# Performance work log

Hardware: AMD Instinct MI355X
Metric: run time of the kernel (lower is better)

## Reference

```python
import jax, jax.numpy as jnp
import numpy as np

# Production-scale dims (see shape_source)
B, C, H, W = 4, 128, 64, 64
RADIUS = 0.2
TEMP = 0.1
PAD_VALUE = 0.0
P = int(H * RADIUS) * 2 + 1  # local window size kH = kW = 25


def setup_inputs() -> dict:
    key = jax.random.key(0)
    k1, k2 = jax.random.split(key)
    query = jax.random.normal(k1, (B, C, H, W), dtype=jnp.float32)
    keys = jax.random.normal(k2, (B, C, H, W), dtype=jnp.float32)
    return {"query": query, "keys": keys}


def _make_idx_map(h_dim, w_dim, p):
    # Equivalent of F.unfold(arange(H*W).view(H,W), kernel=(P,P), pad=P//2).clamp(min=0)
    # idx[h, w, p1, p2] = linear index of (h+p1-P//2, w+p2-P//2), 0 if out of bounds
    off = np.arange(p) - p // 2
    hh = np.arange(h_dim)[:, None, None, None] + off[None, None, :, None]  # (H,1,P,1)
    ww = np.arange(w_dim)[None, :, None, None] + off[None, None, None, :]  # (1,W,1,P)
    valid = (hh >= 0) & (hh < h_dim) & (ww >= 0) & (ww < w_dim)
    idx = np.where(valid, hh * w_dim + ww, 0)  # (H,W,P,P)
    return jnp.asarray(idx.reshape(h_dim * w_dim, p * p), dtype=jnp.int32)

_IDX_MAP = _make_idx_map(H, W, P)  # (H*W, P*P) int32 constant


def _local_correlation(query, keys, p):
    # spatial_correlation_sample(kernel=1, patch=P, stride=1, pad=0, dilation=1):
    # att[b,p1,p2,h,w] = sum_c query[b,c,h,w] * keys_zero_padded[b,c,h+p1-P//2,w+p2-P//2]
    pad = p // 2
    keys_pad = jnp.pad(keys, ((0, 0), (0, 0), (pad, pad), (pad, pad)))

    def corr_one(i):
        p1, p2 = i // p, i % p
        k = jax.lax.dynamic_slice(keys_pad, (0, 0, p1, p2), keys.shape)
        return jnp.einsum('bchw,bchw->bhw', query, k)

    att = jax.lax.map(corr_one, jnp.arange(p * p))  # (P*P, B, H, W); sequential keeps memory low
    return jnp.transpose(att, (1, 2, 3, 0))  # b h w (p1 p2)


def reference(query, keys):
    n_pix = H * W
    att = _local_correlation(query, keys, P) / TEMP  # (B,H,W,P*P)
    # knn(): pad_value==0, topk==0 -> mask exact zeros (out-of-window zero-padded corrs) to -10
    A = jnp.where(att == PAD_VALUE, jnp.float32(-10.0), att)
    A = jnp.exp(A.reshape(B, n_pix, P * P))  # b (h w) n
    # scatter_add into dense (B, H*W, H*W) affinity map
    q_idx = jnp.arange(n_pix)[:, None]  # (HW,1)
    out = jnp.zeros((B, n_pix, n_pix), dtype=A.dtype)
    out = out.at[:, q_idx, _IDX_MAP].add(A)
    # rearr 'b (h w) n -> b n h w'
    return out.reshape(B, H, W, n_pix).transpose(0, 3, 1, 2)
```

## Files before the change

kernel.cpp:

```cpp
#include <hip/hip_runtime.h>
#include <math.h>


#define BDIM 256
constexpr int Bn = 4, Cc = 128, Hh = 64, Ww = 64, HW = 4096;
constexpr int P = 25, Rr = 12, T = 8;

__device__ __forceinline__ int cntf(int x) {
    int c = P;
    if (x < Rr) c -= (Rr - x);
    if (x > (Hh - 1 - Rr)) c -= (x - (Hh - 1 - Rr));
    return c;
}

__global__ __launch_bounds__(BDIM, 6) void localwalk_kernel(
    const float* __restrict__ query, const float* __restrict__ keys,
    float* __restrict__ out)
{
    const int jt = blockIdx.x;
    const int jh = blockIdx.y;
    const int b  = blockIdx.z;
    const int jw0 = jt * T;
    const int t = threadIdx.x;

    __shared__ float S[T * P * P];

    const float E10 = expf(-10.0f);
    const bool special = (jh == 0) && (jt == 0);

    const float* kb = keys + (size_t)b * Cc * HW + jh * Ww + jw0;
    for (int i = t; i < Cc * T; i += BDIM)
        S[i] = kb[(size_t)(i >> 3) * HW + (i & 7)];
    __syncthreads();

    const int wg   = t & 7;
    const int hloc = t >> 3;
    const int h  = jh - Rr + hloc;
    const int hA = min(max(h, 0), Hh - 1);
    const int w0 = jw0 - Rr + wg * 4;
    const int wA0 = min(max(w0, 0), Ww - 4);
    const bool wgv = (w0 >= 0) && (w0 + 3 < Ww);
    const bool hok = (hloc < P) && (h >= 0) && (h < Hh);

    float acc[4][T];
    #pragma unroll
    for (int ww = 0; ww < 4; ++ww)
        #pragma unroll
        for (int jj = 0; jj < T; ++jj) acc[ww][jj] = 0.f;

    const float* qp = query + (size_t)b * Cc * HW + hA * Ww + wA0;

#define STEPQ(QREG, CIDX) do {                                            \
        float4 k0_ = *(const float4*)&S[(CIDX) * 8];                      \
        float4 k1_ = *(const float4*)&S[(CIDX) * 8 + 4];                  \
        float kk_[T] = {k0_.x, k0_.y, k0_.z, k0_.w,                       \
                        k1_.x, k1_.y, k1_.z, k1_.w};                      \
        float qq_[4] = {(QREG).x, (QREG).y, (QREG).z, (QREG).w};          \
        _Pragma("unroll")                                                 \
        for (int jj_ = 0; jj_ < T; ++jj_)                                 \
            _Pragma("unroll")                                             \
            for (int ww_ = 0; ww_ < 4; ++ww_)                             \
                acc[ww_][jj_] = fmaf(qq_[ww_], kk_[jj_], acc[ww_][jj_]);  \
    } while (0)
#define LOADQ(QREG, CIDX) (QREG) = *(const float4*)(qp + (size_t)(CIDX) * HW)

    float4 q0, q1, q2, q3;
    LOADQ(q0, 0); LOADQ(q1, 1); LOADQ(q2, 2); LOADQ(q3, 3);

    for (int c0 = 0; c0 < Cc - 4; c0 += 4) {
        STEPQ(q0, c0 + 0); LOADQ(q0, c0 + 4);
        STEPQ(q1, c0 + 1); LOADQ(q1, c0 + 5);
        STEPQ(q2, c0 + 2); LOADQ(q2, c0 + 6);
        STEPQ(q3, c0 + 3); LOADQ(q3, c0 + 7);
    }
    STEPQ(q0, Cc - 4); STEPQ(q1, Cc - 3); STEPQ(q2, Cc - 2); STEPQ(q3, Cc - 1);

#undef STEPQ
#undef LOADQ

    __syncthreads();

    if (hok && wgv) {
        #pragma unroll
        for (int jj = 0; jj < T; ++jj) {
            #pragma unroll
            for (int ww = 0; ww < 4; ++ww) {
                const int d = wg * 4 + ww - jj;
                if ((unsigned)d < (unsigned)P) {
                    float att = acc[ww][jj] / 0.1f;
                    if (att == 0.0f) att = -10.0f;
                    att = fminf(att, 88.0f);
                    S[(jj * P + hloc) * P + d] = expf(att);
                }
            }
        }
    }
    __syncthreads();

    float4* orow4 = (float4*)(out + ((size_t)(b * HW + jh * Ww + jw0)) * HW);
    for (int k = 0; k < 32; ++k) {
        int fi = t + k * BDIM;
        int jj  = fi >> 10;
        int idx = fi & 1023;
        int hh  = idx >> 4;
        int w4  = (idx & 15) * 4;
        int hl  = hh - (jh - Rr);
        bool hin = (hl >= 0) && (hl < P);

        float4 v = make_float4(0.f, 0.f, 0.f, 0.f);
        if (special && jj == 0) {
            int ch = cntf(hh);
            v.x = (float)(P * P - ch * cntf(w4 + 0)) * E10;
            v.y = (float)(P * P - ch * cntf(w4 + 1)) * E10;
            v.z = (float)(P * P - ch * cntf(w4 + 2)) * E10;
            v.w = (float)(P * P - ch * cntf(w4 + 3)) * E10;
        }
        if (hin) {
            int base = (jj * P + hl) * P;
            int off  = jw0 + jj - Rr;
            int we0  = w4 - off;
            if ((unsigned)(we0 + 0) < (unsigned)P) v.x += S[base + we0 + 0];
            if ((unsigned)(we0 + 1) < (unsigned)P) v.y += S[base + we0 + 1];
            if ((unsigned)(we0 + 2) < (unsigned)P) v.z += S[base + we0 + 2];
            if ((unsigned)(we0 + 3) < (unsigned)P) v.w += S[base + we0 + 3];
        }
        orow4[fi] = v;
    }
}

extern "C" void kernel_launch(void* const* d_in, const int* in_sizes, int n_in,
                              void* d_out, int out_size, void* d_ws, size_t ws_size,
                              hipStream_t stream) {
    const float* query = (const float*)d_in[0];
    const float* keys  = (const float*)d_in[1];
    float* out = (float*)d_out;
    dim3 grid(Ww / T, Hh, Bn);
    localwalk_kernel<<<grid, dim3(BDIM), 0, stream>>>(query, keys, out);
}
```

Measured before the change: 354.8 us.

## Process two column tiles per block, overlapping first tile's stores with second tile's compute

Each block now handles 16 query columns as two 8-column tiles. It interleaves the dense output writes of the first tile with the channel-reduction loop of the second tile, so global stores can overlap FMA work. The grid is halved and the occupancy hint drops from 6 to 4. Exchanged for this are more shared memory per block (a key tile buffer of 128×16 floats) and fewer blocks in flight.

```diff
diff --git a/kernel.cpp b/kernel.cpp
--- a/kernel.cpp
+++ b/kernel.cpp
@@ -13,46 +13,69 @@
     return c;
 }
 
-__global__ __launch_bounds__(BDIM, 6) void localwalk_kernel(
+__device__ __forceinline__ void d_chunk(int k, int t, int jh, int jw0s, bool sp,
+                                        const float* __restrict__ S,
+                                        float4* __restrict__ orow4, float E10)
+{
+    int fi  = t + k * BDIM;
+    int jj  = fi >> 10;
+    int idx = fi & 1023;
+    int hh  = idx >> 4;
+    int w4  = (idx & 15) * 4;
+    int hl  = hh - (jh - Rr);
+    bool hin = (hl >= 0) && (hl < P);
+
+    float4 v = make_float4(0.f, 0.f, 0.f, 0.f);
+    if (sp && jj == 0) {
+        int ch = cntf(hh);
+        v.x = (float)(P * P - ch * cntf(w4 + 0)) * E10;
+        v.y = (float)(P * P - ch * cntf(w4 + 1)) * E10;
+        v.z = (float)(P * P - ch * cntf(w4 + 2)) * E10;
+        v.w = (float)(P * P - ch * cntf(w4 + 3)) * E10;
+    }
+    if (hin) {
+        int base = (jj * P + hl) * P;
+        int off  = jw0s + jj - Rr;
+        int we0  = w4 - off;
+        if ((unsigned)(we0 + 0) < (unsigned)P) v.x += S[base + we0 + 0];
+        if ((unsigned)(we0 + 1) < (unsigned)P) v.y += S[base + we0 + 1];
+        if ((unsigned)(we0 + 2) < (unsigned)P) v.z += S[base + we0 + 2];
+        if ((unsigned)(we0 + 3) < (unsigned)P) v.w += S[base + we0 + 3];
+    }
+    orow4[fi] = v;
+}
+
+__global__ __launch_bounds__(BDIM, 4) void localwalk_kernel(
     const float* __restrict__ query, const float* __restrict__ keys,
     float* __restrict__ out)
 {
-    const int jt = blockIdx.x;
+    const int jg = blockIdx.x;
     const int jh = blockIdx.y;
     const int b  = blockIdx.z;
-    const int jw0 = jt * T;
+    const int jwb = jg * 16;
     const int t = threadIdx.x;
 
+    __shared__ float K[Cc * 16];
     __shared__ float S[T * P * P];
 
     const float E10 = expf(-10.0f);
-    const bool special = (jh == 0) && (jt == 0);
 
-    const float* kb = keys + (size_t)b * Cc * HW + jh * Ww + jw0;
-    for (int i = t; i < Cc * T; i += BDIM)
-        S[i] = kb[(size_t)(i >> 3) * HW + (i & 7)];
+    const float* kb = keys + (size_t)b * Cc * HW + jh * Ww + jwb;
+    for (int i = t; i < Cc * 16; i += BDIM)
+        K[i] = kb[(size_t)(i >> 4) * HW + (i & 15)];
     __syncthreads();
 
-    const int wg   = t & 7;
-    const int hloc = t >> 3;
+    const int wg = t & 7, hloc = t >> 3;
     const int h  = jh - Rr + hloc;
     const int hA = min(max(h, 0), Hh - 1);
-    const int w0 = jw0 - Rr + wg * 4;
-    const int wA0 = min(max(w0, 0), Ww - 4);
-    const bool wgv = (w0 >= 0) && (w0 + 3 < Ww);
     const bool hok = (hloc < P) && (h >= 0) && (h < Hh);
+    const float* qbase = query + (size_t)b * Cc * HW + hA * Ww;
 
     float acc[4][T];
-    #pragma unroll
-    for (int ww = 0; ww < 4; ++ww)
-        #pragma unroll
-        for (int jj = 0; jj < T; ++jj) acc[ww][jj] = 0.f;
 
-    const float* qp = query + (size_t)b * Cc * HW + hA * Ww + wA0;
-
-#define STEPQ(QREG, CIDX) do {                                            \
-        float4 k0_ = *(const float4*)&S[(CIDX) * 8];                      \
-        float4 k1_ = *(const float4*)&S[(CIDX) * 8 + 4];                  \
+#define STEPQ(QREG, CIDX, SOFF) do {                                      \
+        float4 k0_ = *(const float4*)&K[(CIDX) * 16 + (SOFF)];            \
+        float4 k1_ = *(const float4*)&K[(CIDX) * 16 + (SOFF) + 4];        \
         float kk_[T] = {k0_.x, k0_.y, k0_.z, k0_.w,                       \
                         k1_.x, k1_.y, k1_.z, k1_.w};                      \
         float qq_[4] = {(QREG).x, (QREG).y, (QREG).z, (QREG).w};          \
@@ -64,67 +87,103 @@
     } while (0)
 #define LOADQ(QREG, CIDX) (QREG) = *(const float4*)(qp + (size_t)(CIDX) * HW)
 
-    float4 q0, q1, q2, q3;
-    LOADQ(q0, 0); LOADQ(q1, 1); LOADQ(q2, 2); LOADQ(q3, 3);
+    {
+        const int jw0 = jwb;
+        const int w0  = jw0 - Rr + wg * 4;
+        const int wA0 = min(max(w0, 0), Ww - 4);
+        const bool wgv = (w0 >= 0) && (w0 + 3 < Ww);
+        const float* qp = qbase + wA0;
 
-    for (int c0 = 0; c0 < Cc - 4; c0 += 4) {
-        STEPQ(q0, c0 + 0); LOADQ(q0, c0 + 4);
-        STEPQ(q1, c0 + 1); LOADQ(q1, c0 + 5);
-        STEPQ(q2, c0 + 2); LOADQ(q2, c0 + 6);
-        STEPQ(q3, c0 + 3); LOADQ(q3, c0 + 7);
-    }
-    STEPQ(q0, Cc - 4); STEPQ(q1, Cc - 3); STEPQ(q2, Cc - 2); STEPQ(q3, Cc - 1);
+        #pragma unroll
+        for (int ww = 0; ww < 4; ++ww)
+            #pragma unroll
+            for (int jj = 0; jj < T; ++jj) acc[ww][jj] = 0.f;
 
-#undef STEPQ
-#undef LOADQ
+        float4 q0, q1, q2, q3;
+        LOADQ(q0, 0); LOADQ(q1, 1); LOADQ(q2, 2); LOADQ(q3, 3);
+        for (int c0 = 0; c0 < Cc - 4; c0 += 4) {
+            STEPQ(q0, c0 + 0, 0); LOADQ(q0, c0 + 4);
+            STEPQ(q1, c0 + 1, 0); LOADQ(q1, c0 + 5);
+            STEPQ(q2, c0 + 2, 0); LOADQ(q2, c0 + 6);
+            STEPQ(q3, c0 + 3, 0); LOADQ(q3, c0 + 7);
+        }
+        STEPQ(q0, Cc - 4, 0); STEPQ(q1, Cc - 3, 0);
+        STEPQ(q2, Cc - 2, 0); STEPQ(q3, Cc - 1, 0);
 
-    __syncthreads();
-
-    if (hok && wgv) {
-        #pragma unroll
-        for (int jj = 0; jj < T; ++jj) {
+        if (hok && wgv) {
             #pragma unroll
-            for (int ww = 0; ww < 4; ++ww) {
-                const int d = wg * 4 + ww - jj;
-                if ((unsigned)d < (unsigned)P) {
-                    float att = acc[ww][jj] / 0.1f;
-                    if (att == 0.0f) att = -10.0f;
-                    att = fminf(att, 88.0f);
-                    S[(jj * P + hloc) * P + d] = expf(att);
+            for (int jj = 0; jj < T; ++jj) {
+                #pragma unroll
+                for (int ww = 0; ww < 4; ++ww) {
+                    const int d = wg * 4 + ww - jj;
+                    if ((unsigned)d < (unsigned)P) {
+                        float att = acc[ww][jj] / 0.1f;
+                        if (att == 0.0f) att = -10.0f;
+                        att = fminf(att, 88.0f);
+                        S[(jj * P + hloc) * P + d] = expf(att);
+                    }
                 }
             }
         }
     }
     __syncthreads();
 
-    float4* orow4 = (float4*)(out + ((size_t)(b * HW + jh * Ww + jw0)) * HW);
-    for (int k = 0; k < 32; ++k) {
-        int fi = t + k * BDIM;
-        int jj  = fi >> 10;
-        int idx = fi & 1023;
-        int hh  = idx >> 4;
-        int w4  = (idx & 15) * 4;
-        int hl  = hh - (jh - Rr);
-        bool hin = (hl >= 0) && (hl < P);
+    {
+        const int jw0 = jwb + T;
+        const int w0  = jw0 - Rr + wg * 4;
+        const int wA0 = min(max(w0, 0), Ww - 4);
+        const bool wgv = (w0 >= 0) && (w0 + 3 < Ww);
+        const float* qp = qbase + wA0;
 
-        float4 v = make_float4(0.f, 0.f, 0.f, 0.f);
-        if (special && jj == 0) {
-            int ch = cntf(hh);
-            v.x = (float)(P * P - ch * cntf(w4 + 0)) * E10;
-            v.y = (float)(P * P - ch * cntf(w4 + 1)) * E10;
-            v.z = (float)(P * P - ch * cntf(w4 + 2)) * E10;
-            v.w = (float)(P * P - ch * cntf(w4 + 3)) * E10;
+        const bool sp0 = (jh == 0) && (jwb == 0);
+        float4* orow0 = (float4*)(out + ((size_t)(b * HW + jh * Ww + jwb)) * HW);
+
+        #pragma unroll
+        for (int ww = 0; ww < 4; ++ww)
+            #pragma unroll
+            for (int jj = 0; jj < T; ++jj) acc[ww][jj] = 0.f;
+
+        float4 q0, q1, q2, q3;
+        LOADQ(q0, 0); LOADQ(q1, 1); LOADQ(q2, 2); LOADQ(q3, 3);
+        for (int c0 = 0; c0 < Cc - 4; c0 += 4) {
+            STEPQ(q0, c0 + 0, 8); LOADQ(q0, c0 + 4);
+            STEPQ(q1, c0 + 1, 8); LOADQ(q1, c0 + 5);
+            STEPQ(q2, c0 + 2, 8); LOADQ(q2, c0 + 6);
+            STEPQ(q3, c0 + 3, 8); LOADQ(q3, c0 + 7);
+            d_chunk(c0 >> 2, t, jh, jwb, sp0, S, orow0, E10);
         }
-        if (hin) {
-            int base = (jj * P + hl) * P;
-            int off  = jw0 + jj - Rr;
-            int we0  = w4 - off;
-            if ((unsigned)(we0 + 0) < (unsigned)P) v.x += S[base + we0 + 0];
-            if ((unsigned)(we0 + 1) < (unsigned)P) v.y += S[base + we0 + 1];
-            if ((unsigned)(we0 + 2) < (unsigned)P) v.z += S[base + we0 + 2];
-            if ((unsigned)(we0 + 3) < (unsigned)P) v.w += S[base + we0 + 3];
+        STEPQ(q0, Cc - 4, 8); STEPQ(q1, Cc - 3, 8);
+        STEPQ(q2, Cc - 2, 8); STEPQ(q3, Cc - 1, 8);
+        d_chunk(31, t, jh, jwb, sp0, S, orow0, E10);
+
+        __syncthreads();
+
+        if (hok && wgv) {
+            #pragma unroll
+            for (int jj = 0; jj < T; ++jj) {
+                #pragma unroll
+                for (int ww = 0; ww < 4; ++ww) {
+                    const int d = wg * 4 + ww - jj;
+                    if ((unsigned)d < (unsigned)P) {
+                        float att = acc[ww][jj] / 0.1f;
+                        if (att == 0.0f) att = -10.0f;
+                        att = fminf(att, 88.0f);
+                        S[(jj * P + hloc) * P + d] = expf(att);
+                    }
+                }
+            }
         }
-        orow4[fi] = v;
+    }
+    __syncthreads();
+
+#undef STEPQ
+#undef LOADQ
+
+    {
+        const int jw01 = jwb + T;
+        float4* orow1 = (float4*)(out + ((size_t)(b * HW + jh * Ww + jw01)) * HW);
+        for (int k = 0; k < 32; ++k)
+            d_chunk(k, t, jh, jw01, false, S, orow1, E10);
     }
 }
 
@@ -134,6 +193,6 @@
     const float* query = (const float*)d_in[0];
     const float* keys  = (const float*)d_in[1];
     float* out = (float*)d_out;
-    dim3 grid(Ww / T, Hh, Bn);
+    dim3 grid(Ww / (T * 2), Hh, Bn);
     localwalk_kernel<<<grid, dim3(BDIM), 0, stream>>>(query, keys, out);
 }
```

Result: faster. 327.6 us, median of 2 (-7.6%).
